# Optimization experiments

Hardware: AMD Instinct MI355X
Metric: run time of the kernel (lower is better)

Reference implementation:

```python
import jax, jax.numpy as jnp
import numpy as np

L, D, H, FF, I, MAXREL = 6, 512, 8, 2048, 50, 128
HD = D // H
NREL = 2 * MAXREL + 1
EPS = 1e-5


def setup_inputs() -> dict:
    key = jax.random.key(0)
    ks = jax.random.split(key, 32)
    s = 0.02
    p = {
        'x': jax.random.normal(ks[0], (16, 512, I), dtype=jnp.float32),
        'in_w': jax.random.normal(ks[1], (I, D)) * s,
        'in_b': jnp.zeros((D,), jnp.float32),
        'Wq': jax.random.normal(ks[2], (L, D, D)) * s,
        'Wk': jax.random.normal(ks[3], (L, D, D)) * s,
        'Wv': jax.random.normal(ks[4], (L, D, D)) * s,
        'Wo': jax.random.normal(ks[5], (L, D, D)) * s,
        'bo': jnp.zeros((L, D), jnp.float32),
        'rel_emb': jax.random.normal(ks[6], (L, NREL, HD)) * s,
        'w1': jax.random.normal(ks[7], (L, D, FF)) * s,
        'b1': jnp.zeros((L, FF), jnp.float32),
        'w2': jax.random.normal(ks[8], (L, FF, D)) * s,
        'b2': jnp.zeros((L, D), jnp.float32),
        'ln1_g': jnp.ones((L, D), jnp.float32),
        'ln1_b': jnp.zeros((L, D), jnp.float32),
        'ln2_g': jnp.ones((L, D), jnp.float32),
        'ln2_b': jnp.zeros((L, D), jnp.float32),
        'on_g': jnp.ones((D,), jnp.float32),
        'on_b': jnp.zeros((D,), jnp.float32),
        'p1_w': jax.random.normal(ks[9], (D, D // 2)) * s,
        'p1_b': jnp.zeros((D // 2,), jnp.float32),
        'p2_w': jax.random.normal(ks[10], (D // 2, 1)) * s,
        'p2_b': jnp.zeros((1,), jnp.float32),
    }
    return p


def _layer_norm(x, g, b):
    m = jnp.mean(x, axis=-1, keepdims=True)
    v = jnp.mean(jnp.square(x - m), axis=-1, keepdims=True)
    return (x - m) * jax.lax.rsqrt(v + EPS) * g + b


def _sinusoidal_pe(seq_len, d_model):
    pos = jnp.arange(seq_len, dtype=jnp.float32)[:, None]
    div = jnp.exp(jnp.arange(0, d_model, 2, dtype=jnp.float32) * (-jnp.log(10000.0) / d_model))
    pe = jnp.zeros((seq_len, d_model), jnp.float32)
    pe = pe.at[:, 0::2].set(jnp.sin(pos * div))
    pe = pe.at[:, 1::2].set(jnp.cos(pos * div))
    return pe


def reference(x, in_w, in_b, Wq, Wk, Wv, Wo, bo, rel_emb, w1, b1, w2, b2,
              ln1_g, ln1_b, ln2_g, ln2_b, on_g, on_b, p1_w, p1_b, p2_w, p2_b):
    B, S, _ = x.shape
    scale = jnp.sqrt(jnp.float32(HD))
    # relative position index matrix [S, S] in [0, 2*MAXREL]
    r = jnp.arange(S)
    rel_idx = jnp.clip(r[None, :] - r[:, None], -MAXREL, MAXREL) + MAXREL

    h = x @ in_w + in_b                       # [B,S,D]
    h = h + _sinusoidal_pe(S, D)

    for l in range(L):
        q = (h @ Wq[l]).reshape(B, S, H, HD).transpose(0, 2, 1, 3)  # [B,H,S,hd]
        k = (h @ Wk[l]).reshape(B, S, H, HD).transpose(0, 2, 1, 3)
        v = (h @ Wv[l]).reshape(B, S, H, HD).transpose(0, 2, 1, 3)
        scores = jnp.einsum('bhqd,bhkd->bhqk', q, k) / scale
        rel = rel_emb[l][rel_idx]             # [S,S,hd]
        scores = scores + jnp.einsum('bhqd,qkd->bhqk', q, rel)  # rel bias is NOT scaled (matches source)
        attn = jax.nn.softmax(scores, axis=-1)
        ctx = jnp.einsum('bhqk,bhkd->bhqd', attn, v)
        ctx = ctx.transpose(0, 2, 1, 3).reshape(B, S, D)
        attn_out = ctx @ Wo[l] + bo[l]
        h = _layer_norm(h + attn_out, ln1_g[l], ln1_b[l])
        ff = jax.nn.relu(h @ w1[l] + b1[l]) @ w2[l] + b2[l]
        h = _layer_norm(h + ff, ln2_g[l], ln2_b[l])

    h = _layer_norm(h, on_g, on_b)
    out = jax.nn.relu(h @ p1_w + p1_b) @ p2_w + p2_b  # [B,S,1]
    return out
```

## Files before the change

kernel.cpp:

```cpp
#include <hip/hip_runtime.h>

typedef unsigned short u16;
typedef unsigned int   u32;
typedef short   short8  __attribute__((ext_vector_type(8)));
typedef float   floatx4 __attribute__((ext_vector_type(4)));

#define NTOK 8192
#define SEQ  512
#define NLAYER 6

#define OFF_WT   ((size_t)0)
#define OFF_HB   ((size_t)38010880)
#define OFF_QKV  ((size_t)46399488)
#define OFF_CTX  ((size_t)71565312)
#define OFF_GOUT ((size_t)79953920)
#define OFF_FF   ((size_t)96731136)
#define OFF_HD1  ((size_t)130285568)
#define OFF_VT   OFF_FF
#define OFF_RELB OFF_HD1

#define LSTRIDE 3145728
#define P1T_OFF 18874368

__device__ __forceinline__ float b2f(u16 v) { return __uint_as_float(((u32)v) << 16); }
__device__ __forceinline__ float lo16(u32 v) { return __uint_as_float(v << 16); }
__device__ __forceinline__ float hi16(u32 v) { return __uint_as_float(v & 0xffff0000u); }
__device__ __forceinline__ u16 f2b(float f) {
  u32 x = __float_as_uint(f);
  return (u16)((x + 0x7fffu + ((x >> 16) & 1u)) >> 16);
}
__device__ __forceinline__ u32 pack2(float a, float b) {
  return (u32)f2b(a) | ((u32)f2b(b) << 16);
}

typedef __attribute__((address_space(1))) void* gas_t;
typedef __attribute__((address_space(3))) void* las_t;

__global__ __launch_bounds__(256) void transpose_all(
    const float* __restrict__ Wq, const float* __restrict__ Wk,
    const float* __restrict__ Wv, const float* __restrict__ Wo,
    const float* __restrict__ w1, const float* __restrict__ w2,
    const float* __restrict__ p1, u16* __restrict__ wT)
{
  __shared__ u16 tile[64][65];
  const int tb = blockIdx.x;
  const float* src; u16* dst; int R, C, tidx;
  if (tb < 4608) {
    const int l = tb / 768, r = tb % 768;
    const size_t lofs = (size_t)l * LSTRIDE;
    if (r < 256) {
      const int m = r >> 6; tidx = r & 63; R = 512; C = 512;
      const float* bases[4] = {Wq, Wk, Wv, Wo};
      src = bases[m] + (size_t)l * 262144;
      dst = wT + lofs + (size_t)m * 262144;
    } else if (r < 512) {
      tidx = r - 256; R = 512; C = 2048;
      src = w1 + (size_t)l * 1048576; dst = wT + lofs + 1048576;
    } else {
      tidx = r - 512; R = 2048; C = 512;
      src = w2 + (size_t)l * 1048576; dst = wT + lofs + 2097152;
    }
  } else {
    tidx = tb - 4608; R = 512; C = 256;
    src = p1; dst = wT + P1T_OFF;
  }
  const int tcn = C >> 6;
  const int tr = tidx / tcn, tc = tidx % tcn;
  const int th = threadIdx.x;
  {
    const int lr = th >> 2, cg = (th & 3) * 16;
    const float* sp = src + (size_t)(tr*64 + lr) * C + tc*64 + cg;
    float4 f0 = *(const float4*)(sp);
    float4 f1 = *(const float4*)(sp + 4);
    float4 f2 = *(const float4*)(sp + 8);
    float4 f3 = *(const float4*)(sp + 12);
    u16* tp = &tile[lr][cg];
    tp[0]=f2b(f0.x); tp[1]=f2b(f0.y); tp[2]=f2b(f0.z); tp[3]=f2b(f0.w);
    tp[4]=f2b(f1.x); tp[5]=f2b(f1.y); tp[6]=f2b(f1.z); tp[7]=f2b(f1.w);
    tp[8]=f2b(f2.x); tp[9]=f2b(f2.y); tp[10]=f2b(f2.z); tp[11]=f2b(f2.w);
    tp[12]=f2b(f3.x); tp[13]=f2b(f3.y); tp[14]=f2b(f3.z); tp[15]=f2b(f3.w);
  }
  __syncthreads();
  {
    const int oc = th >> 2, rg = (th & 3) * 16;
    u32 wds[8];
    #pragma unroll
    for (int i = 0; i < 8; ++i)
      wds[i] = (u32)tile[rg + 2*i][oc] | ((u32)tile[rg + 2*i + 1][oc] << 16);
    u16* dp = dst + (size_t)(tc*64 + oc) * R + tr*64 + rg;
    uint4 o0; o0.x=wds[0]; o0.y=wds[1]; o0.z=wds[2]; o0.w=wds[3];
    uint4 o1; o1.x=wds[4]; o1.y=wds[5]; o1.z=wds[6]; o1.w=wds[7];
    *(uint4*)dp = o0;
    *(uint4*)(dp + 8) = o1;
  }
}

__global__ __launch_bounds__(128) void input_proj(
    const float* __restrict__ x, const float* __restrict__ w, const float* __restrict__ ib,
    u16* __restrict__ hb)
{
  const int row = blockIdx.x, t = threadIdx.x;
  const int s = row & (SEQ - 1);
  __shared__ float xs[50];
  if (t < 50) xs[t] = x[row*50 + t];
  __syncthreads();
  #pragma unroll
  for (int rep = 0; rep < 4; ++rep) {
    const int d = rep*128 + t;
    float acc = ib[d];
    #pragma unroll
    for (int i = 0; i < 50; ++i) acc += xs[i] * w[i*512 + d];
    const int ii = d >> 1;
    const float dv = __expf((float)(2*ii) * -0.017988946f);
    const float ang = (float)s * dv;
    const float pe = (d & 1) ? cosf(ang) : sinf(ang);
    hb[(size_t)row*512 + d] = f2b(acc + pe);
  }
}

__global__ __launch_bounds__(256) void gemm_bt(
    const u16* __restrict__ A, const u16* __restrict__ Bt,
    const float* __restrict__ bias,
    float* __restrict__ outF0, float* __restrict__ outF1, u16* __restrict__ outB,
    u16* __restrict__ vTout,
    const int M, const int N, const int K, const int kLen, const int flags)
{
  __shared__ __align__(16) u16 As[2*128*32];
  __shared__ __align__(16) u16 Bs[2*128*32];
  const int id = blockIdx.x;
  const int xcd = id & 7, rest = id >> 3;
  const int bm = (rest & 7) * 8 + xcd;
  const int bn = rest >> 3;
  const int z = blockIdx.y;
  const int kOff = z * kLen;
  const int m0 = bm << 7, n0 = bn << 7;
  const int tid = threadIdx.x;
  const int wave = tid >> 6, lane = tid & 63;
  const int wr = (wave >> 1) << 6, wc = (wave & 1) << 6;
  const int lrow = lane & 15, lquad = lane >> 4;

  floatx4 acc[4][4];
  #pragma unroll
  for (int i = 0; i < 4; ++i)
    #pragma unroll
    for (int j = 0; j < 4; ++j) { floatx4 zz = {0.f,0.f,0.f,0.f}; acc[i][j] = zz; }

  const u16* a0p = A  + (size_t)m0 * K + kOff;
  const u16* b0p = Bt + (size_t)n0 * K + kOff;
  const int c0 = tid, c1 = 256 + tid;
  const int ar0 = c0 >> 2, as0 = (c0 & 3) * 8;
  const int ar1 = c1 >> 2, as1 = (c1 & 3) * 8;

  for (int k0 = 0; k0 < kLen; k0 += 64) {
    #pragma unroll
    for (int hh = 0; hh < 2; ++hh) {
      const int kk = k0 + hh*32;
      __builtin_amdgcn_global_load_lds((gas_t)(a0p + (size_t)ar0*K + kk + as0), (las_t)(&As[hh*4096 + c0*8]), 16, 0, 0);
      __builtin_amdgcn_global_load_lds((gas_t)(a0p + (size_t)ar1*K + kk + as1), (las_t)(&As[hh*4096 + c1*8]), 16, 0, 0);
      __builtin_amdgcn_global_load_lds((gas_t)(b0p + (size_t)ar0*K + kk + as0), (las_t)(&Bs[hh*4096 + c0*8]), 16, 0, 0);
      __builtin_amdgcn_global_load_lds((gas_t)(b0p + (size_t)ar1*K + kk + as1), (las_t)(&Bs[hh*4096 + c1*8]), 16, 0, 0);
    }
    __syncthreads();
    #pragma unroll
    for (int hh = 0; hh < 2; ++hh) {
      short8 af[4], bf[4];
      #pragma unroll
      for (int i = 0; i < 4; ++i) af[i] = *(const short8*)&As[hh*4096 + (wr + i*16 + lrow)*32 + lquad*8];
      #pragma unroll
      for (int j = 0; j < 4; ++j) bf[j] = *(const short8*)&Bs[hh*4096 + (wc + j*16 + lrow)*32 + lquad*8];
      #pragma unroll
      for (int i = 0; i < 4; ++i)
        #pragma unroll
        for (int j = 0; j < 4; ++j)
          acc[i][j] = __builtin_amdgcn_mfma_f32_16x16x32_bf16(bf[j], af[i], acc[i][j], 0, 0, 0);
    }
    __syncthreads();
  }

  if ((flags & 4) && n0 >= 1024) {
    #pragma unroll
    for (int i = 0; i < 4; ++i) {
      const int row = m0 + wr + i*16 + lrow;
      const int bb = row >> 9, s = row & 511;
      #pragma unroll
      for (int j = 0; j < 4; ++j) {
        const int cm0 = (n0 - 1024) + wc + j*16 + lquad*4;
        #pragma unroll
        for (int v = 0; v < 4; ++v) {
          const int cm = cm0 + v;
          const int hh = cm >> 6, d = cm & 63;
          vTout[((size_t)(bb*8 + hh)*64 + d)*512 + s] = f2b(acc[i][j][v]);
        }
      }
    }
    return;
  }

  float* outF = (z == 0) ? outF0 : outF1;
  const bool hasb = ((flags & 1) != 0) && (z == 0);
  const bool dorelu = (flags & 2) != 0;
  #pragma unroll
  for (int i = 0; i < 4; ++i) {
    const int row = m0 + wr + i*16 + lrow;
    #pragma unroll
    for (int j = 0; j < 4; ++j) {
      const int colbase = n0 + wc + j*16 + lquad*4;
      float4 bv4 = make_float4(0.f, 0.f, 0.f, 0.f);
      if (hasb) bv4 = *(const float4*)(bias + colbase);
      float v0 = acc[i][j][0] + bv4.x;
      float v1 = acc[i][j][1] + bv4.y;
      float v2 = acc[i][j][2] + bv4.z;
      float v3 = acc[i][j][3] + bv4.w;
      if (dorelu) {
        v0 = fmaxf(v0, 0.f); v1 = fmaxf(v1, 0.f);
        v2 = fmaxf(v2, 0.f); v3 = fmaxf(v3, 0.f);
      }
      const size_t off = (size_t)row * N + colbase;
      if (outB) {
        uint2 o; o.x = pack2(v0, v1); o.y = pack2(v2, v3);
        *(uint2*)(outB + off) = o;
      } else {
        *(float4*)(outF + off) = make_float4(v0, v1, v2, v3);
      }
    }
  }
}

__global__ __launch_bounds__(256) void cvt_rel_all(
    const float* __restrict__ rel, u16* __restrict__ relB)
{
  const int i = blockIdx.x*256 + threadIdx.x;
  if (i < 6*257*64) {
    const int l = i / 16448, rem = i % 16448;
    relB[l*17408 + rem] = f2b(rel[i]);
  }
}

__global__ __launch_bounds__(256, 3) void attn_mfma(
    const u16* __restrict__ qkv, const u16* __restrict__ vT,
    const u16* __restrict__ relB, u16* __restrict__ ctx)
{
  const int id = blockIdx.x;
  const int xcd = id & 7, g = (id >> 3) & 15, qt = id >> 7;
  const int bh = xcd*16 + g;
  const int b = bh >> 3, h = bh & 7;
  const int t = threadIdx.x, w = t >> 6, lane = t & 63;
  const int lr = lane & 15, quad = lane >> 4;

  __shared__ __align__(16) u16 Ks[64*72];
  __shared__ __align__(16) u16 Vs[64*72];
  __shared__ __align__(16) u16 Pr[64*272];

  const size_t token0 = (size_t)b*512 + qt*64;
  const int srow = t >> 2, scol = (t & 3) * 16;
  const u16* kbase = qkv + (size_t)b*512*1536 + 512 + h*64;
  const u16* vbase = vT + (size_t)bh*64*512;

  short8 af0, af1;
  {
    const u16* qp = qkv + (token0 + w*16 + lr)*1536 + h*64 + quad*8;
    af0 = *(const short8*)(qp);
    af1 = *(const short8*)(qp + 32);
  }

  uint4 kr0, kr1, vr0, vr1;
  {
    const u16* kp = kbase + (size_t)srow*1536 + scol;
    kr0 = *(const uint4*)kp; kr1 = *(const uint4*)(kp + 8);
    const u16* vp = vbase + (size_t)srow*512 + scol;
    vr0 = *(const uint4*)vp; vr1 = *(const uint4*)(vp + 8);
  }

  #pragma unroll 4
  for (int nt = 0; nt < 17; ++nt) {
    const u16* rp = relB + (nt*16 + lr)*64 + quad*8;
    short8 rb0 = *(const short8*)(rp);
    short8 rb1 = *(const short8*)(rp + 32);
    floatx4 c = {0.f,0.f,0.f,0.f};
    c = __builtin_amdgcn_mfma_f32_16x16x32_bf16(af0, rb0, c, 0, 0, 0);
    c = __builtin_amdgcn_mfma_f32_16x16x32_bf16(af1, rb1, c, 0, 0, 0);
    #pragma unroll
    for (int r = 0; r < 4; ++r)
      Pr[(w*16 + quad*4 + r)*272 + nt*16 + lr] = f2b(c[r] * 1.44269504f);
  }

  floatx4 oacc[4];
  floatx4 lacc = {0.f,0.f,0.f,0.f};
  #pragma unroll
  for (int n = 0; n < 4; ++n) { floatx4 zz = {0.f,0.f,0.f,0.f}; oacc[n] = zz; }

  short8 ones;
  #pragma unroll
  for (int i = 0; i < 8; ++i) ones[i] = (short)0x3F80;

  const int qg0 = qt*64 + w*16 + quad*4;
  const int prrow0 = (w*16 + quad*4)*272;
  const int psrow0 = (w*16 + quad*4)*72;

  for (int kt = 0; kt < 8; ++kt) {
    __syncthreads();
    *(uint4*)&Ks[srow*72 + scol]     = kr0;
    *(uint4*)&Ks[srow*72 + scol + 8] = kr1;
    *(uint4*)&Vs[srow*72 + scol]     = vr0;
    *(uint4*)&Vs[srow*72 + scol + 8] = vr1;
    __syncthreads();

    if (kt < 7) {
      const u16* kp = kbase + (size_t)((kt+1)*64 + srow)*1536 + scol;
      kr0 = *(const uint4*)kp; kr1 = *(const uint4*)(kp + 8);
      const u16* vp = vbase + (size_t)srow*512 + (kt+1)*64 + scol;
      vr0 = *(const uint4*)vp; vr1 = *(const uint4*)(vp + 8);
    }

    floatx4 s4[4];
    __builtin_amdgcn_s_setprio(1);
    #pragma unroll
    for (int nt = 0; nt < 4; ++nt) {
      short8 kb0 = *(const short8*)&Ks[(nt*16 + lr)*72 + quad*8];
      short8 kb1 = *(const short8*)&Ks[(nt*16 + lr)*72 + 32 + quad*8];
      floatx4 c = {0.f,0.f,0.f,0.f};
      c = __builtin_amdgcn_mfma_f32_16x16x32_bf16(af0, kb0, c, 0, 0, 0);
      c = __builtin_amdgcn_mfma_f32_16x16x32_bf16(af1, kb1, c, 0, 0, 0);
      s4[nt] = c;
    }
    __builtin_amdgcn_s_setprio(0);
    __syncthreads();

    const int kpos = kt*64 + lr;
    #pragma unroll
    for (int r = 0; r < 4; ++r) {
      const int qg = qg0 + r;
      const int prrow = prrow0 + r*272;
      const int psrow = psrow0 + r*72;
      #pragma unroll
      for (int nt = 0; nt < 4; ++nt) {
        int dd = (kpos + nt*16) - qg;
        dd = dd < -128 ? -128 : (dd > 128 ? 128 : dd);
        const float sc = fmaf(s4[nt][r], 0.18033688f, b2f(Pr[prrow + dd + 128]));
        Ks[psrow + nt*16 + lr] = f2b(exp2f(sc));
      }
    }

    short8 pf0 = *(const short8*)&Ks[(w*16 + lr)*72 + quad*8];
    short8 pf1 = *(const short8*)&Ks[(w*16 + lr)*72 + 32 + quad*8];
    __builtin_amdgcn_s_setprio(1);
    lacc = __builtin_amdgcn_mfma_f32_16x16x32_bf16(ones, pf0, lacc, 0, 0, 0);
    lacc = __builtin_amdgcn_mfma_f32_16x16x32_bf16(ones, pf1, lacc, 0, 0, 0);
    #pragma unroll
    for (int nd = 0; nd < 4; ++nd) {
      short8 vb0 = *(const short8*)&Vs[(nd*16 + lr)*72 + quad*8];
      short8 vb1 = *(const short8*)&Vs[(nd*16 + lr)*72 + 32 + quad*8];
      oacc[nd] = __builtin_amdgcn_mfma_f32_16x16x32_bf16(vb0, pf0, oacc[nd], 0, 0, 0);
      oacc[nd] = __builtin_amdgcn_mfma_f32_16x16x32_bf16(vb1, pf1, oacc[nd], 0, 0, 0);
    }
    __builtin_amdgcn_s_setprio(0);
  }

  {
    const float inv = 1.f / lacc[0];
    u16* cp = ctx + (token0 + w*16 + lr)*512 + h*64;
    #pragma unroll
    for (int nd = 0; nd < 4; ++nd) {
      const int d = nd*16 + quad*4;
      uint2 o;
      o.x = pack2(oacc[nd][0]*inv, oacc[nd][1]*inv);
      o.y = pack2(oacc[nd][2]*inv, oacc[nd][3]*inv);
      *(uint2*)(cp + d) = o;
    }
  }
}

__global__ __launch_bounds__(128) void ln_kernel(
    const u16* __restrict__ resB, const float* __restrict__ add0,
    const float* __restrict__ add1,
    const float* __restrict__ g, const float* __restrict__ be,
    u16* __restrict__ hb)
{
  const int row = blockIdx.x, t = threadIdx.x;
  const size_t base = (size_t)row * 512;
  const u32 r0 = *(const u32*)(resB + base + t*4);
  const u32 r1 = *(const u32*)(resB + base + t*4 + 2);
  float x0 = lo16(r0), x1 = hi16(r0), x2 = lo16(r1), x3 = hi16(r1);
  if (add0) {
    const float4 a = *(const float4*)(add0 + base + t*4);
    x0 += a.x; x1 += a.y; x2 += a.z; x3 += a.w;
  }
  if (add1) {
    const float4 a = *(const float4*)(add1 + base + t*4);
    x0 += a.x; x1 += a.y; x2 += a.z; x3 += a.w;
  }
  float s = x0 + x1 + x2 + x3;
  #pragma unroll
  for (int off = 32; off > 0; off >>= 1) s += __shfl_down(s, off);
  __shared__ float red[2];
  const int wv = t >> 6, ln = t & 63;
  if (ln == 0) red[wv] = s;
  __syncthreads();
  const float mean = (red[0] + red[1]) * (1.f/512.f);
  const float dx0 = x0-mean, dx1 = x1-mean, dx2 = x2-mean, dx3 = x3-mean;
  float vs = dx0*dx0 + dx1*dx1 + dx2*dx2 + dx3*dx3;
  __syncthreads();
  #pragma unroll
  for (int off = 32; off > 0; off >>= 1) vs += __shfl_down(vs, off);
  if (ln == 0) red[wv] = vs;
  __syncthreads();
  const float var = (red[0] + red[1]) * (1.f/512.f);
  const float inv = 1.f / sqrtf(var + 1e-5f);
  const float4 gv = *(const float4*)(g + t*4);
  const float4 bv = *(const float4*)(be + t*4);
  const float y0 = dx0*inv*gv.x + bv.x;
  const float y1 = dx1*inv*gv.y + bv.y;
  const float y2 = dx2*inv*gv.z + bv.z;
  const float y3 = dx3*inv*gv.w + bv.w;
  u32* hp = (u32*)(hb + base + t*4);
  hp[0] = pack2(y0, y1); hp[1] = pack2(y2, y3);
}

__global__ __launch_bounds__(256) void head2_kernel(
    const u16* __restrict__ hd1, const float* __restrict__ p2w,
    const float* __restrict__ p2b, float* __restrict__ out)
{
  const int wv = threadIdx.x >> 6, ln = threadIdx.x & 63;
  const int row = blockIdx.x * 4 + wv;
  const u16* hp = hd1 + (size_t)row * 256 + ln*4;
  const u32 h0 = *(const u32*)hp, h1 = *(const u32*)(hp + 2);
  const float4 w = *(const float4*)(p2w + ln*4);
  float acc = lo16(h0)*w.x + hi16(h0)*w.y + lo16(h1)*w.z + hi16(h1)*w.w;
  #pragma unroll
  for (int off = 1; off < 64; off <<= 1) acc += __shfl_xor(acc, off);
  if (ln == 0) out[row] = acc + p2b[0];
}

extern "C" void kernel_launch(void* const* d_in, const int* in_sizes, int n_in,
                              void* d_out, int out_size, void* d_ws, size_t ws_size,
                              hipStream_t stream) {
  (void)in_sizes; (void)n_in; (void)out_size; (void)ws_size;
  const float* X    = (const float*)d_in[0];
  const float* INW  = (const float*)d_in[1];
  const float* INB  = (const float*)d_in[2];
  const float* WQ   = (const float*)d_in[3];
  const float* WK   = (const float*)d_in[4];
  const float* WV   = (const float*)d_in[5];
  const float* WO   = (const float*)d_in[6];
  const float* BO   = (const float*)d_in[7];
  const float* REL  = (const float*)d_in[8];
  const float* W1   = (const float*)d_in[9];
  const float* B1   = (const float*)d_in[10];
  const float* W2   = (const float*)d_in[11];
  const float* B2   = (const float*)d_in[12];
  const float* LN1G = (const float*)d_in[13];
  const float* LN1B = (const float*)d_in[14];
  const float* LN2G = (const float*)d_in[15];
  const float* LN2B = (const float*)d_in[16];
  const float* ONG  = (const float*)d_in[17];
  const float* ONB  = (const float*)d_in[18];
  const float* P1W  = (const float*)d_in[19];
  const float* P1B  = (const float*)d_in[20];
  const float* P2W  = (const float*)d_in[21];
  const float* P2B  = (const float*)d_in[22];
  float* out = (float*)d_out;

  char* ws = (char*)d_ws;
  u16*   wT    = (u16*)(ws + OFF_WT);
  u16*   hB    = (u16*)(ws + OFF_HB);
  u16*   qkv   = (u16*)(ws + OFF_QKV);
  u16*   ctx   = (u16*)(ws + OFF_CTX);
  float* gout0 = (float*)(ws + OFF_GOUT);
  float* gout1 = (float*)(ws + OFF_QKV);
  u16*   ff    = (u16*)(ws + OFF_FF);
  u16*   hd1   = (u16*)(ws + OFF_HD1);
  u16*   vTb   = (u16*)(ws + OFF_VT);
  u16*   relBa = (u16*)(ws + OFF_RELB);

  transpose_all<<<4640, 256, 0, stream>>>(WQ, WK, WV, WO, W1, W2, P1W, wT);
  cvt_rel_all<<<386, 256, 0, stream>>>(REL, relBa);
  input_proj<<<NTOK, 128, 0, stream>>>(X, INW, INB, hB);

  for (int l = 0; l < NLAYER; ++l) {
    const u16* wTl = wT + (size_t)l * LSTRIDE;
    gemm_bt<<<dim3(768,1), 256, 0, stream>>>(hB, wTl, nullptr, nullptr, nullptr, qkv, vTb,
                                             8192, 1536, 512, 512, 4);
    attn_mfma<<<1024, 256, 0, stream>>>(qkv, vTb, relBa + l*17408, ctx);
    gemm_bt<<<dim3(256,2), 256, 0, stream>>>(ctx, wTl + 786432, BO + l*512,
                                             gout0, gout1, nullptr, nullptr,
                                             8192, 512, 512, 256, 1);
    ln_kernel<<<NTOK, 128, 0, stream>>>(hB, gout0, gout1, LN1G + l*512, LN1B + l*512, hB);
    gemm_bt<<<dim3(1024,1), 256, 0, stream>>>(hB, wTl + 1048576, B1 + l*2048,
                                              nullptr, nullptr, ff, nullptr,
                                              8192, 2048, 512, 512, 3);
    gemm_bt<<<dim3(256,2), 256, 0, stream>>>(ff, wTl + 2097152, B2 + l*512,
                                             gout0, gout1, nullptr, nullptr,
                                             8192, 512, 2048, 1024, 1);
    ln_kernel<<<NTOK, 128, 0, stream>>>(hB, gout0, gout1, LN2G + l*512, LN2B + l*512, hB);
  }
  ln_kernel<<<NTOK, 128, 0, stream>>>(hB, nullptr, nullptr, ONG, ONB, hB);
  gemm_bt<<<dim3(128,1), 256, 0, stream>>>(hB, wT + P1T_OFF, P1B,
                                           nullptr, nullptr, hd1, nullptr,
                                           8192, 256, 512, 512, 3);
  head2_kernel<<<2048, 256, 0, stream>>>(hd1, P2W, P2B, out);
}
```

Before: 1.178 ms.

## Keep attention probabilities in registers instead of round-tripping through LDS

New measurement: 1.141 ms. 1.03x faster.

```diff
diff --git a/kernel.cpp b/kernel.cpp
--- a/kernel.cpp
+++ b/kernel.cpp
@@ -4,6 +4,7 @@
 typedef unsigned int   u32;
 typedef short   short8  __attribute__((ext_vector_type(8)));
 typedef float   floatx4 __attribute__((ext_vector_type(4)));
+typedef int     intx4   __attribute__((ext_vector_type(4)));
 
 #define NTOK 8192
 #define SEQ  512
@@ -31,6 +32,11 @@
 }
 __device__ __forceinline__ u32 pack2(float a, float b) {
   return (u32)f2b(a) | ((u32)f2b(b) << 16);
+}
+__device__ __forceinline__ u32 cvtpk(float a, float b) {
+  u32 r;
+  asm("v_cvt_pk_bf16_f32 %0, %1, %2" : "=v"(r) : "v"(a), "v"(b));
+  return r;
 }
 
 typedef __attribute__((address_space(1))) void* gas_t;
@@ -249,7 +255,7 @@
 
   __shared__ __align__(16) u16 Ks[64*72];
   __shared__ __align__(16) u16 Vs[64*72];
-  __shared__ __align__(16) u16 Pr[64*272];
+  __shared__ __align__(16) u16 Pr[64*274];
 
   const size_t token0 = (size_t)b*512 + qt*64;
   const int srow = t >> 2, scol = (t & 3) * 16;
@@ -281,21 +287,16 @@
     c = __builtin_amdgcn_mfma_f32_16x16x32_bf16(af1, rb1, c, 0, 0, 0);
     #pragma unroll
     for (int r = 0; r < 4; ++r)
-      Pr[(w*16 + quad*4 + r)*272 + nt*16 + lr] = f2b(c[r] * 1.44269504f);
+      Pr[(w*16 + quad*4 + r)*274 + nt*16 + lr] = f2b(c[r] * 1.44269504f);
   }
 
   floatx4 oacc[4];
-  floatx4 lacc = {0.f,0.f,0.f,0.f};
+  float lacc = 0.f;
   #pragma unroll
   for (int n = 0; n < 4; ++n) { floatx4 zz = {0.f,0.f,0.f,0.f}; oacc[n] = zz; }
 
-  short8 ones;
-  #pragma unroll
-  for (int i = 0; i < 8; ++i) ones[i] = (short)0x3F80;
-
-  const int qg0 = qt*64 + w*16 + quad*4;
-  const int prrow0 = (w*16 + quad*4)*272;
-  const int psrow0 = (w*16 + quad*4)*72;
+  const int qglob = qt*64 + w*16 + lr;
+  const int prbase = (w*16 + lr)*274 + 128;
 
   for (int kt = 0; kt < 8; ++kt) {
     __syncthreads();
@@ -319,45 +320,59 @@
       short8 kb0 = *(const short8*)&Ks[(nt*16 + lr)*72 + quad*8];
       short8 kb1 = *(const short8*)&Ks[(nt*16 + lr)*72 + 32 + quad*8];
       floatx4 c = {0.f,0.f,0.f,0.f};
-      c = __builtin_amdgcn_mfma_f32_16x16x32_bf16(af0, kb0, c, 0, 0, 0);
-      c = __builtin_amdgcn_mfma_f32_16x16x32_bf16(af1, kb1, c, 0, 0, 0);
+      c = __builtin_amdgcn_mfma_f32_16x16x32_bf16(kb0, af0, c, 0, 0, 0);
+      c = __builtin_amdgcn_mfma_f32_16x16x32_bf16(kb1, af1, c, 0, 0, 0);
       s4[nt] = c;
     }
     __builtin_amdgcn_s_setprio(0);
-    __syncthreads();
-
-    const int kpos = kt*64 + lr;
-    #pragma unroll
-    for (int r = 0; r < 4; ++r) {
-      const int qg = qg0 + r;
-      const int prrow = prrow0 + r*272;
-      const int psrow = psrow0 + r*72;
+
+    u32 wq[4][2];
+    const int kq = kt*64 + quad*4 - qglob;
+    #pragma unroll
+    for (int nt = 0; nt < 4; ++nt) {
+      const int dbase = kq + nt*16;
+      float p[4];
       #pragma unroll
-      for (int nt = 0; nt < 4; ++nt) {
-        int dd = (kpos + nt*16) - qg;
+      for (int r = 0; r < 4; ++r) {
+        int dd = dbase + r;
         dd = dd < -128 ? -128 : (dd > 128 ? 128 : dd);
-        const float sc = fmaf(s4[nt][r], 0.18033688f, b2f(Pr[prrow + dd + 128]));
-        Ks[psrow + nt*16 + lr] = f2b(exp2f(sc));
+        p[r] = exp2f(fmaf(s4[nt][r], 0.18033688f, b2f(Pr[prbase + dd])));
       }
-    }
-
-    short8 pf0 = *(const short8*)&Ks[(w*16 + lr)*72 + quad*8];
-    short8 pf1 = *(const short8*)&Ks[(w*16 + lr)*72 + 32 + quad*8];
+      lacc += (p[0] + p[1]) + (p[2] + p[3]);
+      wq[nt][0] = cvtpk(p[0], p[1]);
+      wq[nt][1] = cvtpk(p[2], p[3]);
+    }
+
+    intx4 pw0; pw0.x = (int)wq[0][0]; pw0.y = (int)wq[0][1];
+               pw0.z = (int)wq[1][0]; pw0.w = (int)wq[1][1];
+    intx4 pw1; pw1.x = (int)wq[2][0]; pw1.y = (int)wq[2][1];
+               pw1.z = (int)wq[3][0]; pw1.w = (int)wq[3][1];
+    const short8 pf0 = __builtin_bit_cast(short8, pw0);
+    const short8 pf1 = __builtin_bit_cast(short8, pw1);
+
     __builtin_amdgcn_s_setprio(1);
-    lacc = __builtin_amdgcn_mfma_f32_16x16x32_bf16(ones, pf0, lacc, 0, 0, 0);
-    lacc = __builtin_amdgcn_mfma_f32_16x16x32_bf16(ones, pf1, lacc, 0, 0, 0);
     #pragma unroll
     for (int nd = 0; nd < 4; ++nd) {
-      short8 vb0 = *(const short8*)&Vs[(nd*16 + lr)*72 + quad*8];
-      short8 vb1 = *(const short8*)&Vs[(nd*16 + lr)*72 + 32 + quad*8];
+      const int vrow = (nd*16 + lr)*72;
+      uint2 a0 = *(const uint2*)&Vs[vrow + quad*4];
+      uint2 a1 = *(const uint2*)&Vs[vrow + 16 + quad*4];
+      uint2 a2 = *(const uint2*)&Vs[vrow + 32 + quad*4];
+      uint2 a3 = *(const uint2*)&Vs[vrow + 48 + quad*4];
+      intx4 v0; v0.x = (int)a0.x; v0.y = (int)a0.y; v0.z = (int)a1.x; v0.w = (int)a1.y;
+      intx4 v1; v1.x = (int)a2.x; v1.y = (int)a2.y; v1.z = (int)a3.x; v1.w = (int)a3.y;
+      const short8 vb0 = __builtin_bit_cast(short8, v0);
+      const short8 vb1 = __builtin_bit_cast(short8, v1);
       oacc[nd] = __builtin_amdgcn_mfma_f32_16x16x32_bf16(vb0, pf0, oacc[nd], 0, 0, 0);
       oacc[nd] = __builtin_amdgcn_mfma_f32_16x16x32_bf16(vb1, pf1, oacc[nd], 0, 0, 0);
     }
     __builtin_amdgcn_s_setprio(0);
   }
 
+  lacc += __shfl_xor(lacc, 16);
+  lacc += __shfl_xor(lacc, 32);
+
   {
-    const float inv = 1.f / lacc[0];
+    const float inv = 1.f / lacc;
     u16* cp = ctx + (token0 + w*16 + lr)*512 + h*64;
     #pragma unroll
     for (int nd = 0; nd < 4; ++nd) {
```
